# Optimization experiments

Hardware: AMD Instinct MI355X
Metric: run time of the kernel (lower is better)

The kernel has to match this reference:

```python
import jax, jax.numpy as jnp
import numpy as np

B, T, D_IN, H_ENC, LAT = 8192, 256, 17, 32, 8
H_DEC = D_IN  # decoder nn.LSTM(hidden_dim=32 -> input_dim=17)


def _glorot(key, shape, fan):
    bound = 1.0 / np.sqrt(fan)
    return jax.random.uniform(key, shape, jnp.float32, -bound, bound)


def setup_inputs() -> dict:
    key = jax.random.key(0)
    ks = jax.random.split(key, 13)
    x = jax.random.normal(ks[0], (B, T, D_IN), jnp.float32)
    # encoder LSTM params (PyTorch layout: [4H, in], gate order i,f,g,o)
    Wih_e = _glorot(ks[1], (4 * H_ENC, D_IN), H_ENC)
    Whh_e = _glorot(ks[2], (4 * H_ENC, H_ENC), H_ENC)
    bih_e = _glorot(ks[3], (4 * H_ENC,), H_ENC)
    bhh_e = _glorot(ks[4], (4 * H_ENC,), H_ENC)
    # enc_fc / dec_fc
    W_encfc = _glorot(ks[5], (LAT, H_ENC), H_ENC)
    b_encfc = _glorot(ks[6], (LAT,), H_ENC)
    W_decfc = _glorot(ks[7], (H_ENC, LAT), LAT)
    b_decfc = _glorot(ks[8], (H_ENC,), LAT)
    # decoder LSTM: input size H_ENC=32, hidden size D_IN=17
    Wih_d = _glorot(ks[9], (4 * H_DEC, H_ENC), H_DEC)
    Whh_d = _glorot(ks[10], (4 * H_DEC, H_DEC), H_DEC)
    bih_d = _glorot(ks[11], (4 * H_DEC,), H_DEC)
    bhh_d = _glorot(ks[12], (4 * H_DEC,), H_DEC)
    return dict(x=x, Wih_e=Wih_e, Whh_e=Whh_e, bih_e=bih_e, bhh_e=bhh_e,
                W_encfc=W_encfc, b_encfc=b_encfc, W_decfc=W_decfc, b_decfc=b_decfc,
                Wih_d=Wih_d, Whh_d=Whh_d, bih_d=bih_d, bhh_d=bhh_d)


def _lstm(x, Wih, Whh, bih, bhh, hidden):
    # x: [B,T,I]; returns (outputs [B,T,H], h_final [B,H])
    b = x.shape[0]
    # input contribution precomputed for all timesteps: [T,B,4H]
    xg = (jnp.einsum('bti,gi->btg', x, Wih) + bih + bhh).transpose(1, 0, 2)
    h0 = jnp.zeros((b, hidden), x.dtype)
    c0 = jnp.zeros((b, hidden), x.dtype)

    def step(carry, xt):
        h, c = carry
        gates = xt + h @ Whh.T  # [B,4H]
        i, f, g, o = jnp.split(gates, 4, axis=-1)
        i = jax.nn.sigmoid(i)
        f = jax.nn.sigmoid(f)
        g = jnp.tanh(g)
        o = jax.nn.sigmoid(o)
        c = f * c + i * g
        h = o * jnp.tanh(c)
        return (h, c), h

    (h_fin, _), ys = jax.lax.scan(step, (h0, c0), xg)
    return ys.transpose(1, 0, 2), h_fin


def reference(x, Wih_e, Whh_e, bih_e, bhh_e, W_encfc, b_encfc,
              W_decfc, b_decfc, Wih_d, Whh_d, bih_d, bhh_d):
    _, h = _lstm(x, Wih_e, Whh_e, bih_e, bhh_e, H_ENC)          # h: [B,32]
    z = h @ W_encfc.T + b_encfc                                  # [B,8]
    dec_in = jnp.broadcast_to((z @ W_decfc.T + b_decfc)[:, None, :],
                              (x.shape[0], x.shape[1], H_ENC))   # [B,T,32]
    out, _ = _lstm(dec_in, Wih_d, Whh_d, bih_d, bhh_d, H_DEC)    # [B,T,17]
    return out, z
```

## Files before the change

kernel.cpp:

```cpp
#include <hip/hip_runtime.h>

typedef float f32x4 __attribute__((ext_vector_type(4)));
typedef short short8 __attribute__((ext_vector_type(8)));
typedef short s16x4 __attribute__((ext_vector_type(4)));

#define B_TOT   8192
#define T_STEPS 256
#define D_INP   17
#define OUT0 ((long)B_TOT * T_STEPS * D_INP)
#define L2E 1.4426950408889634f

__device__ __forceinline__ float bf2f(unsigned short u) {
    union { unsigned int i; float f; } v; v.i = ((unsigned int)u) << 16; return v.f;
}
__device__ __forceinline__ unsigned short f2bf(float x) {
    union { float f; unsigned int i; } v; v.f = x;
    unsigned int r = (v.i + 0x7fffu + ((v.i >> 16) & 1u)) >> 16;
    return (unsigned short)r;
}
__device__ __forceinline__ short f2bfs(float x) { return (short)f2bf(x); }

__device__ __forceinline__ float fsig(float x) {
    float t = __builtin_amdgcn_exp2f(-1.4426950408889634f * x);
    return __builtin_amdgcn_rcpf(1.0f + t);
}
__device__ __forceinline__ float ftanh(float x) {
    float t = __builtin_amdgcn_exp2f(-2.8853900817779268f * x);
    return 2.0f * __builtin_amdgcn_rcpf(1.0f + t) - 1.0f;
}

__device__ __forceinline__ unsigned cvtpk(float lo, float hi) {
    unsigned r;
    asm("v_cvt_pk_bf16_f32 %0, %1, %2" : "=v"(r) : "v"(lo), "v"(hi));
    return r;
}

union U2S8 { uint4 u; short8 s; };
union U1S4 { uint2 u; s16x4 s; };

#if __has_builtin(__builtin_amdgcn_mfma_f32_16x16x16bf16_1k)
__device__ __forceinline__ f32x4 mfma16(s16x4 a, s16x4 b, f32x4 c) {
    return __builtin_amdgcn_mfma_f32_16x16x16bf16_1k(a, b, c, 0, 0, 0);
}
#else
__device__ __forceinline__ f32x4 mfma16(s16x4 a, s16x4 b, f32x4 c) {
    f32x4 d;
    asm volatile("v_mfma_f32_16x16x16_bf16 %0, %1, %2, %3\n\t"
                 "s_nop 7\n\ts_nop 7"
                 : "=v"(d) : "v"(a), "v"(b), "v"(c));
    return d;
}
#endif

__device__ __forceinline__ float cell_cnshared(float gi, float gf, float gg, float go,
                                               float& c) {
    const float Ei = __builtin_amdgcn_exp2f(-L2E * gi);
    const float Ef = __builtin_amdgcn_exp2f(-L2E * gf);
    const float Eg = __builtin_amdgcn_exp2f(-2.f * L2E * gg);
    const float pf = 1.f + Ef;
    const float A  = (1.f + Ei) * (1.f + Eg);
    const float cn = (c * A + pf * (1.f - Eg)) * __builtin_amdgcn_rcpf(pf * A);
    c = cn;
    return fsig(go) * ftanh(cn);
}

__global__ __launch_bounds__(64, 1)
void lstm_ae_mfma10(const float* __restrict__ x,
                    const float* __restrict__ wih_e,
                    const float* __restrict__ whh_e,
                    const float* __restrict__ bih_e,
                    const float* __restrict__ bhh_e,
                    const float* __restrict__ w_encfc,
                    const float* __restrict__ b_encfc,
                    const float* __restrict__ w_decfc,
                    const float* __restrict__ b_decfc,
                    const float* __restrict__ wih_d,
                    const float* __restrict__ whh_d,
                    const float* __restrict__ bih_d,
                    const float* __restrict__ bhh_d,
                    float* __restrict__ out)
{
    const int lane = threadIdx.x;
    const int n    = lane & 15;
    const int G    = lane >> 4;
    const int row0 = blockIdx.x * 16;

    __shared__ float hfin[16][33];
    __shared__ float zbuf[16][8];

    short8 Aih[4][2], Awh[4][2];
    f32x4  biasE[4][2];
#pragma unroll
    for (int q = 0; q < 4; ++q) {
#pragma unroll
        for (int j = 0; j < 2; ++j) {
            const int u0   = 8*(n>>2) + 4*j + (n&3);
            const int grow = 32*q + u0;
#pragma unroll
            for (int e = 0; e < 8; ++e) {
                const int k = 8*G + e;
                Awh[q][j][e] = f2bfs(whh_e[grow*32 + k]);
                Aih[q][j][e] = (k < D_INP) ? f2bfs(wih_e[grow*D_INP + k]) : (short)0;
            }
#pragma unroll
            for (int r = 0; r < 4; ++r) {
                const int u = 8*G + 4*j + r;
                biasE[q][j][r] = bih_e[32*q + u] + bhh_e[32*q + u];
            }
        }
    }

    float c[8], hreg[8];
#pragma unroll
    for (int e = 0; e < 8; ++e) { c[e] = 0.f; hreg[e] = 0.f; }
    short8 bh;
#pragma unroll
    for (int e = 0; e < 8; ++e) bh[e] = 0;

    const long xrow = (long)(row0 + n) * (T_STEPS * D_INP);

    float xv[8], xn1[8];
#pragma unroll
    for (int e = 0; e < 8; ++e) {
        const int k = 8*G + e;
        xv[e]  = (k < D_INP) ? x[xrow + k] : 0.f;
        xn1[e] = (k < D_INP) ? x[xrow + D_INP + k] : 0.f;
    }

    for (int t = 0; t < T_STEPS; ++t) {
        const int t2 = (t+2 < T_STEPS) ? (t+2) : (T_STEPS-1);
        float xn2[8];
#pragma unroll
        for (int e = 0; e < 8; ++e) {
            const int k = 8*G + e;
            xn2[e] = (k < D_INP) ? x[xrow + (long)t2*D_INP + k] : 0.f;
        }

        U2S8 bxu;
        bxu.u = make_uint4(cvtpk(xv[0], xv[1]), cvtpk(xv[2], xv[3]),
                           cvtpk(xv[4], xv[5]), cvtpk(xv[6], xv[7]));
        const short8 bx = bxu.s;

        f32x4 a[4][2];
#pragma unroll
        for (int q = 0; q < 4; ++q)
#pragma unroll
            for (int j = 0; j < 2; ++j)
                a[q][j] = __builtin_amdgcn_mfma_f32_16x16x32_bf16(Aih[q][j], bx, biasE[q][j], 0, 0, 0);
#pragma unroll
        for (int q = 0; q < 4; ++q)
#pragma unroll
            for (int j = 0; j < 2; ++j)
                a[q][j] = __builtin_amdgcn_mfma_f32_16x16x32_bf16(Awh[q][j], bh, a[q][j], 0, 0, 0);

#pragma unroll
        for (int j = 0; j < 2; ++j)
#pragma unroll
            for (int r = 0; r < 4; ++r) {
                const int e = 4*j + r;
                const float cn = fsig(a[1][j][r])*c[e] + fsig(a[0][j][r])*ftanh(a[2][j][r]);
                c[e] = cn;
                hreg[e] = fsig(a[3][j][r])*ftanh(cn);
            }

        U2S8 bhu;
        bhu.u = make_uint4(cvtpk(hreg[0], hreg[1]), cvtpk(hreg[2], hreg[3]),
                           cvtpk(hreg[4], hreg[5]), cvtpk(hreg[6], hreg[7]));
        bh = bhu.s;

#pragma unroll
        for (int e = 0; e < 8; ++e) { xv[e] = xn1[e]; xn1[e] = xn2[e]; }
    }

#pragma unroll
    for (int j = 0; j < 2; ++j)
#pragma unroll
        for (int r = 0; r < 4; ++r)
            hfin[n][8*G + 4*j + r] = hreg[4*j + r];
    __syncthreads();

#pragma unroll
    for (int ti = 0; ti < 2; ++ti) {
        const int tk = lane*2 + ti;
        const int nn = tk >> 3;
        const int p  = tk & 7;
        float s = b_encfc[p];
#pragma unroll
        for (int jj = 0; jj < 32; ++jj)
            s += hfin[nn][jj] * w_encfc[p*32 + jj];
        out[OUT0 + (long)(row0+nn)*8 + p] = s;
        zbuf[nn][p] = s;
    }
    __syncthreads();

    short8 bdvH, bdvM;
#pragma unroll
    for (int e = 0; e < 8; ++e) {
        const int k = 8*G + e;
        float v = b_decfc[k];
#pragma unroll
        for (int p = 0; p < 8; ++p)
            v += zbuf[n][p] * w_decfc[k*8 + p];
        const unsigned short hh = f2bf(v);
        bdvH[e] = (short)hh;
        bdvM[e] = f2bfs(v - bf2f(hh));
    }

    s16x4  AwhD16[4];
    s16x4  Awh16;
    f32x4  accd[4];
    f32x4  accd16;
    float  w16colv[4][4];
    float  w1616v[4];
    {
#pragma unroll
        for (int q = 0; q < 4; ++q) {
#pragma unroll
            for (int e = 0; e < 4; ++e) {
                const int k = 4*G + e;
                AwhD16[q][e] = f2bfs(whh_d[(q*17 + n)*17 + k]);
            }
#pragma unroll
            for (int r = 0; r < 4; ++r)
                w16colv[q][r] = whh_d[(q*17 + 4*G + r)*17 + 16];
        }
#pragma unroll
        for (int e = 0; e < 4; ++e) {
            const int k = 4*G + e;
            Awh16[e] = (n < 4) ? f2bfs(whh_d[(n*17 + 16)*17 + k]) : (short)0;
        }
#pragma unroll
        for (int r = 0; r < 4; ++r)
            w1616v[r] = whh_d[(r*17 + 16)*17 + 16];

#pragma unroll
        for (int q = 0; q < 4; ++q) {
            short8 ADH, ADM;
#pragma unroll
            for (int e = 0; e < 8; ++e) {
                const int k = 8*G + e;
                const float iv = wih_d[(q*17 + n)*32 + k];
                const short hi = f2bfs(iv);
                ADH[e] = hi;
                ADM[e] = f2bfs(iv - bf2f((unsigned short)hi));
            }
            f32x4 acc0;
#pragma unroll
            for (int r = 0; r < 4; ++r) {
                const int u = 4*G + r;
                acc0[r] = bih_d[q*17 + u] + bhh_d[q*17 + u];
            }
            acc0 = __builtin_amdgcn_mfma_f32_16x16x32_bf16(ADH, bdvH, acc0, 0, 0, 0);
            acc0 = __builtin_amdgcn_mfma_f32_16x16x32_bf16(ADM, bdvH, acc0, 0, 0, 0);
            acc0 = __builtin_amdgcn_mfma_f32_16x16x32_bf16(ADH, bdvM, acc0, 0, 0, 0);
            accd[q] = acc0;
        }
        {
            short8 A16H, A16M;
#pragma unroll
            for (int e = 0; e < 8; ++e) {
                const int k = 8*G + e;
                const float iv = (n < 4) ? wih_d[(n*17 + 16)*32 + k] : 0.f;
                const short hi = f2bfs(iv);
                A16H[e] = hi;
                A16M[e] = f2bfs(iv - bf2f((unsigned short)hi));
            }
            f32x4 acc0;
#pragma unroll
            for (int r = 0; r < 4; ++r)
                acc0[r] = (G == 0) ? (bih_d[r*17 + 16] + bhh_d[r*17 + 16]) : 0.f;
            acc0 = __builtin_amdgcn_mfma_f32_16x16x32_bf16(A16H, bdvH, acc0, 0, 0, 0);
            acc0 = __builtin_amdgcn_mfma_f32_16x16x32_bf16(A16M, bdvH, acc0, 0, 0, 0);
            acc0 = __builtin_amdgcn_mfma_f32_16x16x32_bf16(A16H, bdvM, acc0, 0, 0, 0);
            accd16 = acc0;
        }
    }

    float cd[4];
#pragma unroll
    for (int r = 0; r < 4; ++r) cd[r] = 0.f;
    float c16 = 0.f, h16b = 0.f;
    s16x4 bh4;
#pragma unroll
    for (int e = 0; e < 4; ++e) bh4[e] = 0;

    const long orow = (long)(row0 + n) * (T_STEPS * D_INP);

    for (int t = 0; t < T_STEPS; ++t) {
        f32x4 d[4];
#pragma unroll
        for (int q = 0; q < 4; ++q)
            d[q] = mfma16(AwhD16[q], bh4, accd[q]);
        f32x4 a16 = mfma16(Awh16, bh4, accd16);

#pragma unroll
        for (int q = 0; q < 4; ++q)
#pragma unroll
            for (int r = 0; r < 4; ++r)
                d[q][r] += w16colv[q][r] * h16b;
#pragma unroll
        for (int r = 0; r < 4; ++r)
            a16[r] += w1616v[r] * h16b;

        float hval[4];
#pragma unroll
        for (int r = 0; r < 4; ++r)
            hval[r] = cell_cnshared(d[0][r], d[1][r], d[2][r], d[3][r], cd[r]);

        U1S4 p;
        p.u = make_uint2(cvtpk(hval[0], hval[1]), cvtpk(hval[2], hval[3]));
        bh4 = p.s;

        const float h16 = cell_cnshared(a16[0], a16[1], a16[2], a16[3], c16);

        {
            union { float f; int i; } s, dgt;
            s.f = h16;
            dgt.i = __builtin_amdgcn_ds_bpermute((lane & 15) << 2, s.i);
            h16b = dgt.f;
        }

        const long ob = orow + (long)t * D_INP;
#pragma unroll
        for (int r = 0; r < 4; ++r)
            out[ob + 4*G + r] = hval[r];
        if (G == 0)
            out[ob + 16] = h16;
    }
}

extern "C" void kernel_launch(void* const* d_in, const int* in_sizes, int n_in,
                              void* d_out, int out_size, void* d_ws, size_t ws_size,
                              hipStream_t stream) {
    (void)in_sizes; (void)n_in; (void)d_ws; (void)ws_size; (void)out_size;
    dim3 grid(B_TOT / 16);
    dim3 block(64);
    hipLaunchKernelGGL(lstm_ae_mfma10, grid, block, 0, stream,
        (const float*)d_in[0],
        (const float*)d_in[1],
        (const float*)d_in[2],
        (const float*)d_in[3],
        (const float*)d_in[4],
        (const float*)d_in[5],
        (const float*)d_in[6],
        (const float*)d_in[7],
        (const float*)d_in[8],
        (const float*)d_in[9],
        (const float*)d_in[10],
        (const float*)d_in[11],
        (const float*)d_in[12],
        (float*)d_out);
}
```

Before: 335.0 us.

## Precompute next-step input MFMAs off critical path, replicate gate-16 rows

The encoder's input-projection MFMAs for step t+1 are now issued after the hidden state is produced, so the recurrent critical path holds only the Whh MFMA followed by the cell update. The encoder cell now uses the shared-exponential cell_cnshared formulation, which needs fewer transcendentals. In the decoder, the 17th-unit weights and biases are replicated across all lane groups, so every lane computes h16 itself and the per-step ds_bpermute broadcast is removed. The cost is some redundant arithmetic, more live registers for xacc, and slightly different rounding in the cell math.

```diff
diff --git a/kernel.cpp b/kernel.cpp
--- a/kernel.cpp
+++ b/kernel.cpp
@@ -65,7 +65,7 @@
 }
 
 __global__ __launch_bounds__(64, 1)
-void lstm_ae_mfma10(const float* __restrict__ x,
+void lstm_ae_mfma11(const float* __restrict__ x,
                     const float* __restrict__ wih_e,
                     const float* __restrict__ whh_e,
                     const float* __restrict__ bih_e,
@@ -127,6 +127,18 @@
         xn1[e] = (k < D_INP) ? x[xrow + D_INP + k] : 0.f;
     }
 
+    f32x4 xacc[4][2];
+    {
+        U2S8 bx0;
+        bx0.u = make_uint4(cvtpk(xv[0], xv[1]), cvtpk(xv[2], xv[3]),
+                           cvtpk(xv[4], xv[5]), cvtpk(xv[6], xv[7]));
+#pragma unroll
+        for (int q = 0; q < 4; ++q)
+#pragma unroll
+            for (int j = 0; j < 2; ++j)
+                xacc[q][j] = __builtin_amdgcn_mfma_f32_16x16x32_bf16(Aih[q][j], bx0.s, biasE[q][j], 0, 0, 0);
+    }
+
     for (int t = 0; t < T_STEPS; ++t) {
         const int t2 = (t+2 < T_STEPS) ? (t+2) : (T_STEPS-1);
         float xn2[8];
@@ -136,37 +148,34 @@
             xn2[e] = (k < D_INP) ? x[xrow + (long)t2*D_INP + k] : 0.f;
         }
 
-        U2S8 bxu;
-        bxu.u = make_uint4(cvtpk(xv[0], xv[1]), cvtpk(xv[2], xv[3]),
-                           cvtpk(xv[4], xv[5]), cvtpk(xv[6], xv[7]));
-        const short8 bx = bxu.s;
-
         f32x4 a[4][2];
 #pragma unroll
         for (int q = 0; q < 4; ++q)
 #pragma unroll
             for (int j = 0; j < 2; ++j)
-                a[q][j] = __builtin_amdgcn_mfma_f32_16x16x32_bf16(Aih[q][j], bx, biasE[q][j], 0, 0, 0);
-#pragma unroll
-        for (int q = 0; q < 4; ++q)
-#pragma unroll
-            for (int j = 0; j < 2; ++j)
-                a[q][j] = __builtin_amdgcn_mfma_f32_16x16x32_bf16(Awh[q][j], bh, a[q][j], 0, 0, 0);
+                a[q][j] = __builtin_amdgcn_mfma_f32_16x16x32_bf16(Awh[q][j], bh, xacc[q][j], 0, 0, 0);
 
 #pragma unroll
         for (int j = 0; j < 2; ++j)
 #pragma unroll
             for (int r = 0; r < 4; ++r) {
                 const int e = 4*j + r;
-                const float cn = fsig(a[1][j][r])*c[e] + fsig(a[0][j][r])*ftanh(a[2][j][r]);
-                c[e] = cn;
-                hreg[e] = fsig(a[3][j][r])*ftanh(cn);
+                hreg[e] = cell_cnshared(a[0][j][r], a[1][j][r], a[2][j][r], a[3][j][r], c[e]);
             }
 
         U2S8 bhu;
         bhu.u = make_uint4(cvtpk(hreg[0], hreg[1]), cvtpk(hreg[2], hreg[3]),
                            cvtpk(hreg[4], hreg[5]), cvtpk(hreg[6], hreg[7]));
         bh = bhu.s;
+
+        U2S8 bxn;
+        bxn.u = make_uint4(cvtpk(xn1[0], xn1[1]), cvtpk(xn1[2], xn1[3]),
+                           cvtpk(xn1[4], xn1[5]), cvtpk(xn1[6], xn1[7]));
+#pragma unroll
+        for (int q = 0; q < 4; ++q)
+#pragma unroll
+            for (int j = 0; j < 2; ++j)
+                xacc[q][j] = __builtin_amdgcn_mfma_f32_16x16x32_bf16(Aih[q][j], bxn.s, biasE[q][j], 0, 0, 0);
 
 #pragma unroll
         for (int e = 0; e < 8; ++e) { xv[e] = xn1[e]; xn1[e] = xn2[e]; }
@@ -224,10 +233,13 @@
             for (int r = 0; r < 4; ++r)
                 w16colv[q][r] = whh_d[(q*17 + 4*G + r)*17 + 16];
         }
-#pragma unroll
-        for (int e = 0; e < 4; ++e) {
-            const int k = 4*G + e;
-            Awh16[e] = (n < 4) ? f2bfs(whh_d[(n*17 + 16)*17 + k]) : (short)0;
+        {
+            const int gq = n & 3;
+#pragma unroll
+            for (int e = 0; e < 4; ++e) {
+                const int k = 4*G + e;
+                Awh16[e] = f2bfs(whh_d[(gq*17 + 16)*17 + k]);
+            }
         }
 #pragma unroll
         for (int r = 0; r < 4; ++r)
@@ -256,11 +268,12 @@
             accd[q] = acc0;
         }
         {
+            const int gq = n & 3;
             short8 A16H, A16M;
 #pragma unroll
             for (int e = 0; e < 8; ++e) {
                 const int k = 8*G + e;
-                const float iv = (n < 4) ? wih_d[(n*17 + 16)*32 + k] : 0.f;
+                const float iv = wih_d[(gq*17 + 16)*32 + k];
                 const short hi = f2bfs(iv);
                 A16H[e] = hi;
                 A16M[e] = f2bfs(iv - bf2f((unsigned short)hi));
@@ -268,7 +281,7 @@
             f32x4 acc0;
 #pragma unroll
             for (int r = 0; r < 4; ++r)
-                acc0[r] = (G == 0) ? (bih_d[r*17 + 16] + bhh_d[r*17 + 16]) : 0.f;
+                acc0[r] = bih_d[r*17 + 16] + bhh_d[r*17 + 16];
             acc0 = __builtin_amdgcn_mfma_f32_16x16x32_bf16(A16H, bdvH, acc0, 0, 0, 0);
             acc0 = __builtin_amdgcn_mfma_f32_16x16x32_bf16(A16M, bdvH, acc0, 0, 0, 0);
             acc0 = __builtin_amdgcn_mfma_f32_16x16x32_bf16(A16H, bdvM, acc0, 0, 0, 0);
@@ -312,13 +325,7 @@
         bh4 = p.s;
 
         const float h16 = cell_cnshared(a16[0], a16[1], a16[2], a16[3], c16);
-
-        {
-            union { float f; int i; } s, dgt;
-            s.f = h16;
-            dgt.i = __builtin_amdgcn_ds_bpermute((lane & 15) << 2, s.i);
-            h16b = dgt.f;
-        }
+        h16b = h16;
 
         const long ob = orow + (long)t * D_INP;
 #pragma unroll
@@ -335,7 +342,7 @@
     (void)in_sizes; (void)n_in; (void)d_ws; (void)ws_size; (void)out_size;
     dim3 grid(B_TOT / 16);
     dim3 block(64);
-    hipLaunchKernelGGL(lstm_ae_mfma10, grid, block, 0, stream,
+    hipLaunchKernelGGL(lstm_ae_mfma11, grid, block, 0, stream,
         (const float*)d_in[0],
         (const float*)d_in[1],
         (const float*)d_in[2],
```

Result: no change. 332.8 us (median of 2 runs) (-0.7%).
